# Performance work log

Hardware: AMD Instinct MI355X
Metric: run time of the kernel (lower is better)

## Reference

```python
import jax, jax.numpy as jnp
import numpy as np

N_NODES = 12288
N_EDGES = 393216
LATENT = 128
EDGE_F = 4


def setup_inputs() -> dict:
    key = jax.random.key(0)
    k1, k2, k3, k4 = jax.random.split(key, 4)
    z = jax.random.normal(k1, (N_NODES, LATENT), dtype=jnp.float32)
    edge_index = jax.random.randint(k2, (2, N_EDGES), 0, N_NODES, dtype=jnp.int64)
    edge_attr = jax.random.normal(k3, (N_EDGES, EDGE_F), dtype=jnp.float32)
    W = jax.random.normal(k4, (1, 2 * LATENT), dtype=jnp.float32) * (1.0 / np.sqrt(2 * LATENT))
    b = jnp.zeros((1,), dtype=jnp.float32)
    return {"z": z, "edge_index": edge_index, "edge_attr": edge_attr, "W": W, "b": b}


def reference(z, edge_index, edge_attr, W, b):
    # z: [N, D], edge_index: [2, E], edge_attr: [E, F], W: [1, 2D], b: [1]
    num_nodes = z.shape[0]
    row, col = edge_index[0], edge_index[1]
    # gather node embeddings per edge and apply tiny linear: [E, 2D] @ [2D, 1]
    edge_features = jnp.concatenate([z[row], z[col]], axis=1)
    specified_edge_probs = (edge_features @ W.T + b)[:, 0]  # [E]
    # scatter edge probs into dense NxN (indexed assignment, like torch)
    full_edge_probs = jnp.zeros((num_nodes, num_nodes), dtype=z.dtype).at[row, col].set(specified_edge_probs)
    # to_dense_adj scatter-adds edge_attr -> [N, N, F]; sum(dim=3) commutes, so add summed attr
    adj = jnp.zeros((num_nodes, num_nodes), dtype=edge_attr.dtype).at[row, col].add(edge_attr.sum(axis=1))
    return adj + full_edge_probs
```

## Files before the change

kernel.cpp:

```cpp
#include <hip/hip_runtime.h>

#define N_NODES 12288
#define N_EDGES 393216
#define LATENT  128
#define SLOTS   512
#define BCAP    128


__global__ void node_dots(const float* __restrict__ z, const float* __restrict__ W,
                          float* __restrict__ s1, float* __restrict__ s2) {
    int node = (int)((blockIdx.x * blockDim.x + threadIdx.x) >> 6);
    int lane = (int)(threadIdx.x & 63);
    if (node >= N_NODES) return;
    const float* zr = z + (size_t)node * LATENT;
    float a  = zr[lane];
    float bb = zr[lane + 64];
    float p1 = a * W[lane]       + bb * W[lane + 64];
    float p2 = a * W[lane + 128] + bb * W[lane + 192];
    #pragma unroll
    for (int off = 32; off > 0; off >>= 1) {
        p1 += __shfl_down(p1, off, 64);
        p2 += __shfl_down(p2, off, 64);
    }
    if (lane == 0) { s1[node] = p1; s2[node] = p2; }
}

__global__ void bucket_scatter(const int* __restrict__ ei, const float* __restrict__ ea,
                               unsigned int* __restrict__ cnt,
                               unsigned long long* __restrict__ bpack) {
    int e = (int)(blockIdx.x * blockDim.x + threadIdx.x);
    if (e >= N_EDGES) return;
    unsigned int r = (unsigned int)ei[e];
    unsigned int c = (unsigned int)ei[e + N_EDGES];
    float4 a4 = ((const float4*)ea)[e];
    float s = a4.x + a4.y + a4.z + a4.w;
    unsigned int pos = atomicAdd(&cnt[r], 1u);
    bpack[(size_t)r * BCAP + pos] =
        ((unsigned long long)c << 32) | (unsigned long long)__float_as_uint(s);
}

__global__ __launch_bounds__(256) void row_fill(const unsigned int* __restrict__ cnt,
                                                const unsigned long long* __restrict__ bpack,
                                                const float* __restrict__ s1,
                                                const float* __restrict__ s2,
                                                const float* __restrict__ bptr,
                                                float* __restrict__ out) {
    __shared__ unsigned int hcol[SLOTS];
    __shared__ float        hval[SLOTS];
    int r = (int)blockIdx.x;
    int t = (int)threadIdx.x;

    float4* out4 = (float4*)(out + (size_t)r * N_NODES);
    float4 z = make_float4(0.f, 0.f, 0.f, 0.f);
    #pragma unroll
    for (int i = 0; i < 12; i++) out4[t + i * 256] = z;

    for (int i = t; i < SLOTS; i += 256) { hcol[i] = 0u; hval[i] = 0.f; }
    __syncthreads();

    unsigned int deg = cnt[r];
    const unsigned long long* seg = bpack + (size_t)r * BCAP;
    for (unsigned int i = (unsigned int)t; i < deg; i += 256u) {
        unsigned long long p = seg[i];
        unsigned int c = (unsigned int)(p >> 32);
        float v = __uint_as_float((unsigned int)p);
        unsigned int h = (c * 2654435761u) >> (32 - 9);
        for (;;) {
            unsigned int prev = atomicCAS(&hcol[h], 0u, c + 1u);
            if (prev == 0u) {
                v += s1[r] + s2[c] + bptr[0];
                atomicAdd(&hval[h], v);
                break;
            }
            if (prev == c + 1u) { atomicAdd(&hval[h], v); break; }
            h = (h + 1u) & (SLOTS - 1u);
        }
    }
    __syncthreads();

    for (int i = t; i < SLOTS; i += 256)
        if (hcol[i]) out[(size_t)r * N_NODES + (size_t)(hcol[i] - 1u)] = hval[i];
}

extern "C" void kernel_launch(void* const* d_in, const int* in_sizes, int n_in,
                              void* d_out, int out_size, void* d_ws, size_t ws_size,
                              hipStream_t stream) {
    const float* z  = (const float*)d_in[0];
    const int*   ei = (const int*)d_in[1];
    const float* ea = (const float*)d_in[2];
    const float* W  = (const float*)d_in[3];
    const float* b  = (const float*)d_in[4];
    float* out = (float*)d_out;

    char* ws = (char*)d_ws;
    float*              s1    = (float*)(ws + 0);
    float*              s2    = (float*)(ws + 49152);
    unsigned int*       cnt   = (unsigned int*)(ws + 98304);
    unsigned long long* bpack = (unsigned long long*)(ws + 147456);

    hipMemsetAsync(cnt, 0, N_NODES * sizeof(unsigned int), stream);

    node_dots<<<N_NODES / 4, 256, 0, stream>>>(z, W, s1, s2);
    bucket_scatter<<<N_EDGES / 256, 256, 0, stream>>>(ei, ea, cnt, bpack);
    row_fill<<<N_NODES, 256, 0, stream>>>(cnt, bpack, s1, s2, b, out);
}
```

Baseline: 664.0 us.

## Merge dot and bucket kernels; fill four rows per block with bitmap-guided single pass

```diff
diff --git a/kernel.cpp b/kernel.cpp
--- a/kernel.cpp
+++ b/kernel.cpp
@@ -3,40 +3,44 @@
 #define N_NODES 12288
 #define N_EDGES 393216
 #define LATENT  128
-#define SLOTS   512
 #define BCAP    128
+#define ROWS    4
+#define RSLOTS  128
+#define NCHUNK  (N_NODES / 4)
+#define NBMW    (NCHUNK / 32)
+#define DOT_BLOCKS (N_NODES / 4)
+#define BKT_BLOCKS (N_EDGES / 256)
 
 
-__global__ void node_dots(const float* __restrict__ z, const float* __restrict__ W,
-                          float* __restrict__ s1, float* __restrict__ s2) {
-    int node = (int)((blockIdx.x * blockDim.x + threadIdx.x) >> 6);
-    int lane = (int)(threadIdx.x & 63);
-    if (node >= N_NODES) return;
-    const float* zr = z + (size_t)node * LATENT;
-    float a  = zr[lane];
-    float bb = zr[lane + 64];
-    float p1 = a * W[lane]       + bb * W[lane + 64];
-    float p2 = a * W[lane + 128] + bb * W[lane + 192];
-    #pragma unroll
-    for (int off = 32; off > 0; off >>= 1) {
-        p1 += __shfl_down(p1, off, 64);
-        p2 += __shfl_down(p2, off, 64);
+__global__ void dots_and_bucket(const float* __restrict__ z, const float* __restrict__ W,
+                                const int* __restrict__ ei, const float* __restrict__ ea,
+                                float* __restrict__ s1, float* __restrict__ s2,
+                                unsigned int* __restrict__ cnt,
+                                unsigned long long* __restrict__ bpack) {
+    if (blockIdx.x < DOT_BLOCKS) {
+        int node = (int)(blockIdx.x * 4 + (threadIdx.x >> 6));
+        int lane = (int)(threadIdx.x & 63);
+        const float* zr = z + (size_t)node * LATENT;
+        float a  = zr[lane];
+        float bb = zr[lane + 64];
+        float p1 = a * W[lane]       + bb * W[lane + 64];
+        float p2 = a * W[lane + 128] + bb * W[lane + 192];
+        #pragma unroll
+        for (int off = 32; off > 0; off >>= 1) {
+            p1 += __shfl_down(p1, off, 64);
+            p2 += __shfl_down(p2, off, 64);
+        }
+        if (lane == 0) { s1[node] = p1; s2[node] = p2; }
+    } else {
+        int e = (int)((blockIdx.x - DOT_BLOCKS) * 256 + threadIdx.x);
+        unsigned int r = (unsigned int)ei[e];
+        unsigned int c = (unsigned int)ei[e + N_EDGES];
+        float4 a4 = ((const float4*)ea)[e];
+        float s = a4.x + a4.y + a4.z + a4.w;
+        unsigned int pos = atomicAdd(&cnt[r], 1u);
+        bpack[(size_t)r * BCAP + pos] =
+            ((unsigned long long)c << 32) | (unsigned long long)__float_as_uint(s);
     }
-    if (lane == 0) { s1[node] = p1; s2[node] = p2; }
-}
-
-__global__ void bucket_scatter(const int* __restrict__ ei, const float* __restrict__ ea,
-                               unsigned int* __restrict__ cnt,
-                               unsigned long long* __restrict__ bpack) {
-    int e = (int)(blockIdx.x * blockDim.x + threadIdx.x);
-    if (e >= N_EDGES) return;
-    unsigned int r = (unsigned int)ei[e];
-    unsigned int c = (unsigned int)ei[e + N_EDGES];
-    float4 a4 = ((const float4*)ea)[e];
-    float s = a4.x + a4.y + a4.z + a4.w;
-    unsigned int pos = atomicAdd(&cnt[r], 1u);
-    bpack[(size_t)r * BCAP + pos] =
-        ((unsigned long long)c << 32) | (unsigned long long)__float_as_uint(s);
 }
 
 __global__ __launch_bounds__(256) void row_fill(const unsigned int* __restrict__ cnt,
@@ -45,41 +49,70 @@
                                                 const float* __restrict__ s2,
                                                 const float* __restrict__ bptr,
                                                 float* __restrict__ out) {
-    __shared__ unsigned int hcol[SLOTS];
-    __shared__ float        hval[SLOTS];
-    int r = (int)blockIdx.x;
-    int t = (int)threadIdx.x;
+    __shared__ unsigned int hcol[ROWS][RSLOTS];
+    __shared__ float        hval[ROWS][RSLOTS];
+    __shared__ unsigned int bm[ROWS][NBMW];
+    int r0 = (int)blockIdx.x * ROWS;
+    int t  = (int)threadIdx.x;
 
-    float4* out4 = (float4*)(out + (size_t)r * N_NODES);
-    float4 z = make_float4(0.f, 0.f, 0.f, 0.f);
-    #pragma unroll
-    for (int i = 0; i < 12; i++) out4[t + i * 256] = z;
-
-    for (int i = t; i < SLOTS; i += 256) { hcol[i] = 0u; hval[i] = 0.f; }
+    for (int i = t; i < ROWS * RSLOTS; i += 256) {
+        ((unsigned int*)hcol)[i] = 0u;
+        ((float*)hval)[i] = 0.f;
+    }
+    for (int i = t; i < ROWS * NBMW; i += 256) ((unsigned int*)bm)[i] = 0u;
     __syncthreads();
 
-    unsigned int deg = cnt[r];
-    const unsigned long long* seg = bpack + (size_t)r * BCAP;
-    for (unsigned int i = (unsigned int)t; i < deg; i += 256u) {
-        unsigned long long p = seg[i];
-        unsigned int c = (unsigned int)(p >> 32);
-        float v = __uint_as_float((unsigned int)p);
-        unsigned int h = (c * 2654435761u) >> (32 - 9);
-        for (;;) {
-            unsigned int prev = atomicCAS(&hcol[h], 0u, c + 1u);
-            if (prev == 0u) {
-                v += s1[r] + s2[c] + bptr[0];
-                atomicAdd(&hval[h], v);
-                break;
+    float bias = bptr[0];
+    #pragma unroll
+    for (int rr = 0; rr < ROWS; rr++) {
+        int r = r0 + rr;
+        unsigned int deg = cnt[r];
+        float s1b = s1[r] + bias;
+        const unsigned long long* seg = bpack + (size_t)r * BCAP;
+        for (unsigned int i = (unsigned int)t; i < deg; i += 256u) {
+            unsigned long long p = seg[i];
+            unsigned int c = (unsigned int)(p >> 32);
+            float v = __uint_as_float((unsigned int)p);
+            unsigned int h = (c * 2654435761u) >> 25;
+            for (;;) {
+                unsigned int prev = atomicCAS(&hcol[rr][h], 0u, c + 1u);
+                if (prev == 0u) {
+                    v += s1b + s2[c];
+                    atomicAdd(&hval[rr][h], v);
+                    atomicOr(&bm[rr][c >> 7], 1u << ((c >> 2) & 31));
+                    break;
+                }
+                if (prev == c + 1u) { atomicAdd(&hval[rr][h], v); break; }
+                h = (h + 1u) & (RSLOTS - 1u);
             }
-            if (prev == c + 1u) { atomicAdd(&hval[h], v); break; }
-            h = (h + 1u) & (SLOTS - 1u);
         }
     }
     __syncthreads();
 
-    for (int i = t; i < SLOTS; i += 256)
-        if (hcol[i]) out[(size_t)r * N_NODES + (size_t)(hcol[i] - 1u)] = hval[i];
+    #pragma unroll
+    for (int rr = 0; rr < ROWS; rr++) {
+        float4* out4 = (float4*)(out + (size_t)(r0 + rr) * N_NODES);
+        #pragma unroll
+        for (int i = 0; i < 12; i++) {
+            int j = t + i * 256;
+            float4 v = make_float4(0.f, 0.f, 0.f, 0.f);
+            if (bm[rr][j >> 5] & (1u << (j & 31))) {
+                float* vp = (float*)&v;
+                #pragma unroll
+                for (int k = 0; k < 4; k++) {
+                    unsigned int c = ((unsigned int)j << 2) + (unsigned int)k;
+                    unsigned int h = (c * 2654435761u) >> 25;
+                    for (;;) {
+                        unsigned int pc = hcol[rr][h];
+                        if (pc == 0u) break;
+                        if (pc == c + 1u) { vp[k] = hval[rr][h]; break; }
+                        h = (h + 1u) & (RSLOTS - 1u);
+                    }
+                }
+            }
+            out4[j] = v;
+        }
+    }
 }
 
 extern "C" void kernel_launch(void* const* d_in, const int* in_sizes, int n_in,
@@ -99,8 +132,6 @@
     unsigned long long* bpack = (unsigned long long*)(ws + 147456);
 
     hipMemsetAsync(cnt, 0, N_NODES * sizeof(unsigned int), stream);
-
-    node_dots<<<N_NODES / 4, 256, 0, stream>>>(z, W, s1, s2);
-    bucket_scatter<<<N_EDGES / 256, 256, 0, stream>>>(ei, ea, cnt, bpack);
-    row_fill<<<N_NODES, 256, 0, stream>>>(cnt, bpack, s1, s2, b, out);
+    dots_and_bucket<<<DOT_BLOCKS + BKT_BLOCKS, 256, 0, stream>>>(z, W, ei, ea, s1, s2, cnt, bpack);
+    row_fill<<<N_NODES / ROWS, 256, 0, stream>>>(cnt, bpack, s1, s2, b, out);
 }
```

Result: faster. 647.9 us (-2.4%).

## Merge dot and bucket kernels, zero output with memset, patch rows per wavefront

Applied to the files above, without the earlier changes.

```diff
diff --git a/kernel.cpp b/kernel.cpp
--- a/kernel.cpp
+++ b/kernel.cpp
@@ -3,83 +3,82 @@
 #define N_NODES 12288
 #define N_EDGES 393216
 #define LATENT  128
-#define SLOTS   512
 #define BCAP    128
+#define RSLOTS  128
+#define DOT_BLOCKS (N_NODES / 4)
+#define BKT_BLOCKS (N_EDGES / 256)
 
 
-__global__ void node_dots(const float* __restrict__ z, const float* __restrict__ W,
-                          float* __restrict__ s1, float* __restrict__ s2) {
-    int node = (int)((blockIdx.x * blockDim.x + threadIdx.x) >> 6);
-    int lane = (int)(threadIdx.x & 63);
-    if (node >= N_NODES) return;
-    const float* zr = z + (size_t)node * LATENT;
-    float a  = zr[lane];
-    float bb = zr[lane + 64];
-    float p1 = a * W[lane]       + bb * W[lane + 64];
-    float p2 = a * W[lane + 128] + bb * W[lane + 192];
-    #pragma unroll
-    for (int off = 32; off > 0; off >>= 1) {
-        p1 += __shfl_down(p1, off, 64);
-        p2 += __shfl_down(p2, off, 64);
+__global__ void dots_and_bucket(const float* __restrict__ z, const float* __restrict__ W,
+                                const int* __restrict__ ei, const float* __restrict__ ea,
+                                float* __restrict__ s1, float* __restrict__ s2,
+                                unsigned int* __restrict__ cnt,
+                                unsigned long long* __restrict__ bpack) {
+    if (blockIdx.x < DOT_BLOCKS) {
+        int node = (int)(blockIdx.x * 4 + (threadIdx.x >> 6));
+        int lane = (int)(threadIdx.x & 63);
+        const float* zr = z + (size_t)node * LATENT;
+        float a  = zr[lane];
+        float bb = zr[lane + 64];
+        float p1 = a * W[lane]       + bb * W[lane + 64];
+        float p2 = a * W[lane + 128] + bb * W[lane + 192];
+        #pragma unroll
+        for (int off = 32; off > 0; off >>= 1) {
+            p1 += __shfl_down(p1, off, 64);
+            p2 += __shfl_down(p2, off, 64);
+        }
+        if (lane == 0) { s1[node] = p1; s2[node] = p2; }
+    } else {
+        int e = (int)((blockIdx.x - DOT_BLOCKS) * 256 + threadIdx.x);
+        unsigned int r = (unsigned int)ei[e];
+        unsigned int c = (unsigned int)ei[e + N_EDGES];
+        float4 a4 = ((const float4*)ea)[e];
+        float s = a4.x + a4.y + a4.z + a4.w;
+        unsigned int pos = atomicAdd(&cnt[r], 1u);
+        bpack[(size_t)r * BCAP + pos] =
+            ((unsigned long long)c << 32) | (unsigned long long)__float_as_uint(s);
     }
-    if (lane == 0) { s1[node] = p1; s2[node] = p2; }
 }
 
-__global__ void bucket_scatter(const int* __restrict__ ei, const float* __restrict__ ea,
-                               unsigned int* __restrict__ cnt,
-                               unsigned long long* __restrict__ bpack) {
-    int e = (int)(blockIdx.x * blockDim.x + threadIdx.x);
-    if (e >= N_EDGES) return;
-    unsigned int r = (unsigned int)ei[e];
-    unsigned int c = (unsigned int)ei[e + N_EDGES];
-    float4 a4 = ((const float4*)ea)[e];
-    float s = a4.x + a4.y + a4.z + a4.w;
-    unsigned int pos = atomicAdd(&cnt[r], 1u);
-    bpack[(size_t)r * BCAP + pos] =
-        ((unsigned long long)c << 32) | (unsigned long long)__float_as_uint(s);
-}
+__global__ __launch_bounds__(256) void patch_rows(const unsigned int* __restrict__ cnt,
+                                                  const unsigned long long* __restrict__ bpack,
+                                                  const float* __restrict__ s1,
+                                                  const float* __restrict__ s2,
+                                                  const float* __restrict__ bptr,
+                                                  float* __restrict__ out) {
+    __shared__ unsigned int hcol[4][RSLOTS];
+    __shared__ float        hval[4][RSLOTS];
+    int w    = (int)(threadIdx.x >> 6);
+    int lane = (int)(threadIdx.x & 63);
+    int r    = (int)blockIdx.x * 4 + w;
 
-__global__ __launch_bounds__(256) void row_fill(const unsigned int* __restrict__ cnt,
-                                                const unsigned long long* __restrict__ bpack,
-                                                const float* __restrict__ s1,
-                                                const float* __restrict__ s2,
-                                                const float* __restrict__ bptr,
-                                                float* __restrict__ out) {
-    __shared__ unsigned int hcol[SLOTS];
-    __shared__ float        hval[SLOTS];
-    int r = (int)blockIdx.x;
-    int t = (int)threadIdx.x;
-
-    float4* out4 = (float4*)(out + (size_t)r * N_NODES);
-    float4 z = make_float4(0.f, 0.f, 0.f, 0.f);
-    #pragma unroll
-    for (int i = 0; i < 12; i++) out4[t + i * 256] = z;
-
-    for (int i = t; i < SLOTS; i += 256) { hcol[i] = 0u; hval[i] = 0.f; }
+    hcol[w][lane] = 0u; hcol[w][lane + 64] = 0u;
+    hval[w][lane] = 0.f; hval[w][lane + 64] = 0.f;
     __syncthreads();
 
     unsigned int deg = cnt[r];
+    float s1b = s1[r] + bptr[0];
     const unsigned long long* seg = bpack + (size_t)r * BCAP;
-    for (unsigned int i = (unsigned int)t; i < deg; i += 256u) {
+    for (unsigned int i = (unsigned int)lane; i < deg; i += 64u) {
         unsigned long long p = seg[i];
         unsigned int c = (unsigned int)(p >> 32);
         float v = __uint_as_float((unsigned int)p);
-        unsigned int h = (c * 2654435761u) >> (32 - 9);
+        unsigned int h = (c * 2654435761u) >> 25;
         for (;;) {
-            unsigned int prev = atomicCAS(&hcol[h], 0u, c + 1u);
+            unsigned int prev = atomicCAS(&hcol[w][h], 0u, c + 1u);
             if (prev == 0u) {
-                v += s1[r] + s2[c] + bptr[0];
-                atomicAdd(&hval[h], v);
+                v += s1b + s2[c];
+                atomicAdd(&hval[w][h], v);
                 break;
             }
-            if (prev == c + 1u) { atomicAdd(&hval[h], v); break; }
-            h = (h + 1u) & (SLOTS - 1u);
+            if (prev == c + 1u) { atomicAdd(&hval[w][h], v); break; }
+            h = (h + 1u) & (RSLOTS - 1u);
         }
     }
     __syncthreads();
 
-    for (int i = t; i < SLOTS; i += 256)
-        if (hcol[i]) out[(size_t)r * N_NODES + (size_t)(hcol[i] - 1u)] = hval[i];
+    for (int i = lane; i < RSLOTS; i += 64)
+        if (hcol[w][i]) out[(size_t)r * N_NODES + (size_t)(hcol[w][i] - 1u)] = hval[w][i];
 }
 
 extern "C" void kernel_launch(void* const* d_in, const int* in_sizes, int n_in,
@@ -99,8 +98,9 @@
     unsigned long long* bpack = (unsigned long long*)(ws + 147456);
 
     hipMemsetAsync(cnt, 0, N_NODES * sizeof(unsigned int), stream);
+    dots_and_bucket<<<DOT_BLOCKS + BKT_BLOCKS, 256, 0, stream>>>(z, W, ei, ea, s1, s2, cnt, bpack);
 
-    node_dots<<<N_NODES / 4, 256, 0, stream>>>(z, W, s1, s2);
-    bucket_scatter<<<N_EDGES / 256, 256, 0, stream>>>(ei, ea, cnt, bpack);
-    row_fill<<<N_NODES, 256, 0, stream>>>(cnt, bpack, s1, s2, b, out);
+    hipMemsetAsync(d_out, 0, (size_t)out_size * sizeof(float), stream);
+
+    patch_rows<<<N_NODES / 4, 256, 0, stream>>>(cnt, bpack, s1, s2, b, out);
 }
```

After: 663.3 us. Within noise of the previous version (-0.1%).
